# Performance work log

Hardware: AMD Instinct MI355X
Metric: run time of the kernel (lower is better)

The kernel has to match this reference:

```python
import jax, jax.numpy as jnp
import numpy as np

# Model dims (match init_kwargs)
D_MODEL = 512
NUM_EXPERTS = 8
TOP_K = 2
FFN_MULT = 2
HIDDEN = FFN_MULT * D_MODEL
BATCH, SEQ = 4, 2048


def setup_inputs() -> dict:
    key = jax.random.key(0)
    k_x, k_g, k_bg, k_w1, k_w3, k_w2 = jax.random.split(key, 6)
    sd = 1.0 / np.sqrt(D_MODEL).astype(np.float32)
    sh = 1.0 / np.sqrt(HIDDEN).astype(np.float32)
    return {
        "x": jax.random.normal(k_x, (BATCH, SEQ, D_MODEL), dtype=jnp.float32),
        # gate: nn.Linear(d_model, num_experts) with bias
        "Wg": jax.random.normal(k_g, (D_MODEL, NUM_EXPERTS), dtype=jnp.float32) * sd,
        "bg": jax.random.normal(k_bg, (NUM_EXPERTS,), dtype=jnp.float32) * 0.01,
        # stacked per-expert SwiGLU FFN params (no bias, LLaMA-style)
        "W1": jax.random.normal(k_w1, (NUM_EXPERTS, D_MODEL, HIDDEN), dtype=jnp.float32) * sd,
        "W3": jax.random.normal(k_w3, (NUM_EXPERTS, D_MODEL, HIDDEN), dtype=jnp.float32) * sd,
        "W2": jax.random.normal(k_w2, (NUM_EXPERTS, HIDDEN, D_MODEL), dtype=jnp.float32) * sh,
    }


def reference(x, Wg, bg, W1, W3, W2):
    B, S, D = x.shape
    E = Wg.shape[1]
    xt = x.reshape(-1, D)                        # [T, D], T = B*S
    T = xt.shape[0]

    # Router: top-k over experts, softmax over the k selected logits
    logits = xt @ Wg + bg                        # [T, E]
    top_vals, top_idx = jax.lax.top_k(logits, TOP_K)  # [T, K]
    top_probs = jax.nn.softmax(top_vals, axis=-1)     # [T, K]

    # Dense per-(token, expert) combine weight; zero where expert not selected.
    # top-k indices are distinct per token so scatter-add == scatter-set.
    gate_w = jnp.zeros((T, E), dtype=xt.dtype).at[
        jnp.arange(T)[:, None], top_idx
    ].add(top_probs)                              # [T, E]

    # Loop over experts (fixed, small), accumulate weighted expert outputs.
    def body(y, expert):
        w1, w3, w2, g = expert                   # g: [T]
        h = jax.nn.silu(xt @ w1) * (xt @ w3)     # [T, H]
        return y + g[:, None] * (h @ w2), None

    y0 = jnp.zeros_like(xt)
    y, _ = jax.lax.scan(body, y0, (W1, W3, W2, gate_w.T))
    return y.reshape(B, S, D)
```

## Files before the change

kernel.cpp:

```cpp
#include <hip/hip_runtime.h>
#include <hip/hip_bf16.h>

#define TOKENS 8192
#define DM 512
#define NE 8
#define HID 1024
#define NSLOT (TOKENS * 2)
#define NB 32

#define BM 128
#define BN 64
#define BK 64
#define BN2 128
#define MAXTILE 136

typedef __bf16 bf16x8 __attribute__((ext_vector_type(8)));
typedef float floatx4 __attribute__((ext_vector_type(4)));
typedef unsigned short u16x8 __attribute__((ext_vector_type(8)));

__device__ __forceinline__ unsigned short f2bf(float f) {
    union { float f; unsigned u; } c; c.f = f;
    unsigned u = c.u;
    u += 0x7fffu + ((u >> 16) & 1u);
    return (unsigned short)(u >> 16);
}

__device__ __forceinline__ void load16_lds(const void* g, void* l) {
    __builtin_amdgcn_global_load_lds(
        (const __attribute__((address_space(1))) unsigned int*)g,
        (__attribute__((address_space(3))) unsigned int*)l, 16, 0, 0);
}

__global__ void prep_kernel(const float* __restrict__ x, const float* __restrict__ Wg,
                            const float* __restrict__ bg,
                            const float* __restrict__ W1, const float* __restrict__ W3,
                            const float* __restrict__ W2,
                            unsigned short* __restrict__ w1t, unsigned short* __restrict__ w3t,
                            unsigned short* __restrict__ w2t,
                            int* __restrict__ top_idx, float* __restrict__ top_p,
                            unsigned short* __restrict__ xb) {
    if (blockIdx.x < 3072) {
        __shared__ float tile[64][65];
        const int cb = blockIdx.x;
        const int wsel = cb >> 10;
        const float* src; unsigned short* dst; int K, N;
        if (wsel == 0)      { src = W1; dst = w1t; K = DM;  N = HID; }
        else if (wsel == 1) { src = W3; dst = w3t; K = DM;  N = HID; }
        else                { src = W2; dst = w2t; K = HID; N = DM;  }
        const int tkn = (K >> 6) * (N >> 6);
        int b = cb & 1023;
        int e = b / tkn;
        int rem = b % tkn;
        const int tn6 = N >> 6;
        int kt = rem / tn6, nt = rem % tn6;
        int tx = threadIdx.x & 15, ty = threadIdx.x >> 4;
        const float* s = src + ((size_t)(e * K + kt * 64 + ty)) * N + nt * 64 + tx * 4;
        #pragma unroll
        for (int i = 0; i < 4; i++) {
            float4 v = *(const float4*)(s + (size_t)(i * 16) * N);
            float* tr = &tile[ty + i * 16][tx * 4];
            tr[0] = v.x; tr[1] = v.y; tr[2] = v.z; tr[3] = v.w;
        }
        __syncthreads();
        int n = threadIdx.x >> 3;
        int c8 = (threadIdx.x & 7) * 8;
        unsigned short* d = dst + ((size_t)(e * N + nt * 64)) * K + kt * 64;
        #pragma unroll
        for (int i = 0; i < 2; i++) {
            int nn = n + i * 32;
            u16x8 r;
            #pragma unroll
            for (int kk = 0; kk < 8; kk++) r[kk] = f2bf(tile[c8 + kk][nn]);
            *(u16x8*)(d + (size_t)nn * K + c8) = r;
        }
    } else {
        int lane = threadIdx.x & 63, wave = threadIdx.x >> 6;
        int t = (blockIdx.x - 3072) * 4 + wave;
        float acc[NE];
        #pragma unroll
        for (int e = 0; e < NE; e++) acc[e] = 0.f;
        const float* xr = x + (size_t)t * DM;
        unsigned short* xbr = xb + (size_t)t * DM;
        #pragma unroll
        for (int j = 0; j < 8; j++) {
            int d = lane + j * 64;
            float xv = xr[d];
            xbr[d] = f2bf(xv);
            const float4* wr = (const float4*)(Wg + (size_t)d * NE);
            float4 w0 = wr[0], w1 = wr[1];
            acc[0] += xv * w0.x; acc[1] += xv * w0.y; acc[2] += xv * w0.z; acc[3] += xv * w0.w;
            acc[4] += xv * w1.x; acc[5] += xv * w1.y; acc[6] += xv * w1.z; acc[7] += xv * w1.w;
        }
        #pragma unroll
        for (int e = 0; e < NE; e++) {
            float v = acc[e];
            #pragma unroll
            for (int off = 32; off > 0; off >>= 1) v += __shfl_down(v, off, 64);
            acc[e] = v;
        }
        if (lane == 0) {
            float best = -1e30f, second = -1e30f;
            int bi = 0, si = 0;
            #pragma unroll
            for (int e = 0; e < NE; e++) {
                float v = acc[e] + bg[e];
                if (v > best) { second = best; si = bi; best = v; bi = e; }
                else if (v > second) { second = v; si = e; }
            }
            float ex = __expf(second - best);
            float inv = 1.f / (1.f + ex);
            top_idx[t * 2] = bi;  top_idx[t * 2 + 1] = si;
            top_p[t * 2] = inv;   top_p[t * 2 + 1] = ex * inv;
        }
    }
}

__global__ void sortbuild_kernel(const int* __restrict__ top_idx, const float* __restrict__ top_p,
                                 int* __restrict__ counts, int* __restrict__ offsets,
                                 int* __restrict__ rows, float* __restrict__ gates,
                                 int* __restrict__ slot_of) {
    __shared__ int cntAll[NE], cntBef[NE], cur[NE];
    const int b = blockIdx.x, tid = threadIdx.x;
    const int lane = tid & 63;
    if (tid < NE) { cntAll[tid] = 0; cntBef[tid] = 0; }
    __syncthreads();

    unsigned long long aAll = 0ull, aBef = 0ull;
    for (int k = 0; k < TOKENS / 256; k++) {
        int t = k * 256 + tid;
        int2 ei = *(const int2*)(top_idx + (size_t)t * 2);
        unsigned long long inc = (1ull << (ei.x * 8)) + (1ull << (ei.y * 8));
        aAll += inc;
        if (k < b) aBef += inc;
    }
    auto unpackLo = [](unsigned long long a) {
        return ( a        & 0xFFull)        | ((( a >> 8 ) & 0xFFull) << 16)
             | (((a >> 16) & 0xFFull) << 32) | ((( a >> 24) & 0xFFull) << 48);
    };
    auto unpackHi = [](unsigned long long a) {
        return ((a >> 32) & 0xFFull)        | ((( a >> 40) & 0xFFull) << 16)
             | (((a >> 48) & 0xFFull) << 32) | ((( a >> 56) & 0xFFull) << 48);
    };
    unsigned long long sAllLo = unpackLo(aAll), sAllHi = unpackHi(aAll);
    unsigned long long sBefLo = unpackLo(aBef), sBefHi = unpackHi(aBef);
    #pragma unroll
    for (int off = 32; off > 0; off >>= 1) {
        sAllLo += __shfl_down(sAllLo, off, 64);
        sAllHi += __shfl_down(sAllHi, off, 64);
        sBefLo += __shfl_down(sBefLo, off, 64);
        sBefHi += __shfl_down(sBefHi, off, 64);
    }
    if (lane == 0) {
        #pragma unroll
        for (int e = 0; e < 4; e++) {
            atomicAdd(&cntAll[e],     (int)((sAllLo >> (e * 16)) & 0xFFFF));
            atomicAdd(&cntAll[e + 4], (int)((sAllHi >> (e * 16)) & 0xFFFF));
            atomicAdd(&cntBef[e],     (int)((sBefLo >> (e * 16)) & 0xFFFF));
            atomicAdd(&cntBef[e + 4], (int)((sBefHi >> (e * 16)) & 0xFFFF));
        }
    }
    __syncthreads();
    if (tid < NE) {
        int offs = 0;
        for (int ee = 0; ee < tid; ee++) offs += cntAll[ee];
        cur[tid] = offs + cntBef[tid];
        if (b == 0) { counts[tid] = cntAll[tid]; offsets[tid] = offs; }
    }
    __syncthreads();
    const int t = b * 256 + tid;
    #pragma unroll
    for (int k = 0; k < 2; k++) {
        int e = top_idx[t * 2 + k];
        int slot = atomicAdd(&cur[e], 1);
        rows[slot] = t;
        gates[slot] = top_p[t * 2 + k];
        slot_of[t * 2 + k] = slot;
    }
}

__device__ __forceinline__ bool tile_lookup(const int* counts, const int* offsets, int gy,
                                            int& e, int& mt, int& cnt, int& off) {
    int bacc = 0;
    #pragma unroll
    for (int ee = 0; ee < NE; ee++) {
        int c = counts[ee];
        int ntl = (c + BM - 1) >> 7;
        if (gy < bacc + ntl) { e = ee; mt = gy - bacc; cnt = c; off = offsets[ee]; return true; }
        bacc += ntl;
    }
    return false;
}

__global__ __launch_bounds__(256, 4) void gemm1_kernel(
    const unsigned short* __restrict__ xb,
    const unsigned short* __restrict__ w1t,
    const unsigned short* __restrict__ w3t,
    unsigned short* __restrict__ Hb,
    const int* __restrict__ rows, const int* __restrict__ counts,
    const int* __restrict__ offsets) {
    const int lid = blockIdx.x;
    const int xcd = lid & 7;
    const int j = lid >> 3;
    const int gy = xcd * (MAXTILE / 8) + (j >> 4);
    const int nt = j & 15;
    int e, mt, cnt, off;
    if (!tile_lookup(counts, offsets, gy, e, mt, cnt, off)) return;

    __shared__ unsigned short As[BM * BK];
    __shared__ unsigned short B1s[BN * BK];
    __shared__ unsigned short B3s[BN * BK];

    const int tid = threadIdx.x;
    const int lane = tid & 63, wave = tid >> 6;
    const int lrow8 = lane >> 3;
    const int lchunk = (lane & 7) ^ lrow8;

    const unsigned short* a_g[4];
    #pragma unroll
    for (int i = 0; i < 4; i++) {
        int r = (wave * 4 + i) * 8 + lrow8;
        int gr = mt * BM + r;
        int tok = rows[off + (gr < cnt ? gr : 0)];
        a_g[i] = xb + (size_t)tok * DM + lchunk * 8;
    }
    const unsigned short* b1_g[2]; const unsigned short* b3_g[2];
    #pragma unroll
    for (int i = 0; i < 2; i++) {
        int r = (wave * 2 + i) * 8 + lrow8;
        b1_g[i] = w1t + ((size_t)e * HID + nt * BN + r) * DM + lchunk * 8;
        b3_g[i] = w3t + ((size_t)e * HID + nt * BN + r) * DM + lchunk * 8;
    }

    const int l15 = lane & 15, quad = lane >> 4;
    const int sw = l15 & 7;

    floatx4 acc1[2][4], acc3[2][4];
    #pragma unroll
    for (int i = 0; i < 2; i++)
        #pragma unroll
        for (int j2 = 0; j2 < 4; j2++) {
            acc1[i][j2] = (floatx4){0.f, 0.f, 0.f, 0.f};
            acc3[i][j2] = (floatx4){0.f, 0.f, 0.f, 0.f};
        }

    auto stage = [&](int k0) {
        #pragma unroll
        for (int i = 0; i < 4; i++) load16_lds(a_g[i] + k0, &As[(wave * 4 + i) * 512]);
        #pragma unroll
        for (int i = 0; i < 2; i++) {
            load16_lds(b1_g[i] + k0, &B1s[(wave * 2 + i) * 512]);
            load16_lds(b3_g[i] + k0, &B3s[(wave * 2 + i) * 512]);
        }
    };
    auto compute = [&]() {
        #pragma unroll
        for (int kk = 0; kk < 2; kk++) {
            const int qc = kk * 4 + quad;
            const int ch = (qc ^ sw) << 3;
            bf16x8 af[2], bfrag[4];
            #pragma unroll
            for (int mi = 0; mi < 2; mi++)
                af[mi] = *(const bf16x8*)(&As[(wave * 32 + mi * 16 + l15) * 64 + ch]);
            #pragma unroll
            for (int ni = 0; ni < 4; ni++)
                bfrag[ni] = *(const bf16x8*)(&B1s[(ni * 16 + l15) * 64 + ch]);
            #pragma unroll
            for (int mi = 0; mi < 2; mi++)
                #pragma unroll
                for (int ni = 0; ni < 4; ni++)
                    acc1[mi][ni] = __builtin_amdgcn_mfma_f32_16x16x32_bf16(af[mi], bfrag[ni], acc1[mi][ni], 0, 0, 0);
            #pragma unroll
            for (int ni = 0; ni < 4; ni++)
                bfrag[ni] = *(const bf16x8*)(&B3s[(ni * 16 + l15) * 64 + ch]);
            #pragma unroll
            for (int mi = 0; mi < 2; mi++)
                #pragma unroll
                for (int ni = 0; ni < 4; ni++)
                    acc3[mi][ni] = __builtin_amdgcn_mfma_f32_16x16x32_bf16(af[mi], bfrag[ni], acc3[mi][ni], 0, 0, 0);
        }
    };

    const int NI = DM / BK;
    #pragma unroll
    for (int i = 0; i < NI; i++) {
        if (i) __syncthreads();
        stage(i * BK);
        __syncthreads();
        compute();
    }
    #pragma unroll
    for (int mi = 0; mi < 2; mi++) {
        #pragma unroll
        for (int r = 0; r < 4; r++) {
            int mloc = wave * 32 + mi * 16 + quad * 4 + r;
            int gi = mt * BM + mloc;
            if (gi < cnt) {
                size_t rowbase = (size_t)(off + gi) * HID + nt * BN;
                #pragma unroll
                for (int ni = 0; ni < 4; ni++) {
                    float z1 = acc1[mi][ni][r];
                    float z3 = acc3[mi][ni][r];
                    float h = (z1 / (1.f + __expf(-z1))) * z3;
                    Hb[rowbase + ni * 16 + l15] = f2bf(h);
                }
            }
        }
    }
}

__global__ __launch_bounds__(256) void gemm2_kernel(
    const unsigned short* __restrict__ Hb,
    const unsigned short* __restrict__ w2t,
    unsigned short* __restrict__ P,
    const float* __restrict__ gates,
    const int* __restrict__ counts, const int* __restrict__ offsets) {
    const int lid = blockIdx.x;
    const int xcd = lid & 7;
    const int j = lid >> 3;
    const int gy = xcd * (MAXTILE / 8) + (j >> 2);
    const int nt = j & 3;
    int e, mt, cnt, off;
    if (!tile_lookup(counts, offsets, gy, e, mt, cnt, off)) return;

    __shared__ unsigned short As[BM * BK];
    __shared__ unsigned short Bs[BN2 * BK];

    const int tid = threadIdx.x;
    const int lane = tid & 63, wave = tid >> 6;
    const int lrow8 = lane >> 3;
    const int lchunk = (lane & 7) ^ lrow8;

    const unsigned short* a_g[4];
    #pragma unroll
    for (int i = 0; i < 4; i++) {
        int r = (wave * 4 + i) * 8 + lrow8;
        int sl = off + mt * BM + r;
        if (sl >= NSLOT) sl = NSLOT - 1;
        a_g[i] = Hb + (size_t)sl * HID + lchunk * 8;
    }
    const unsigned short* b_g[4];
    #pragma unroll
    for (int i = 0; i < 4; i++) {
        int r = (wave * 4 + i) * 8 + lrow8;
        b_g[i] = w2t + ((size_t)e * DM + nt * BN2 + r) * HID + lchunk * 8;
    }

    const int l15 = lane & 15, quad = lane >> 4;
    const int sw = l15 & 7;

    floatx4 acc[2][8];
    #pragma unroll
    for (int i = 0; i < 2; i++)
        #pragma unroll
        for (int j2 = 0; j2 < 8; j2++) acc[i][j2] = (floatx4){0.f, 0.f, 0.f, 0.f};

    auto stage = [&](int k0) {
        #pragma unroll
        for (int i = 0; i < 4; i++) load16_lds(a_g[i] + k0, &As[(wave * 4 + i) * 512]);
        #pragma unroll
        for (int i = 0; i < 4; i++) load16_lds(b_g[i] + k0, &Bs[(wave * 4 + i) * 512]);
    };
    auto compute = [&]() {
        #pragma unroll
        for (int kk = 0; kk < 2; kk++) {
            const int qc = kk * 4 + quad;
            const int ch = (qc ^ sw) << 3;
            bf16x8 af[2], bf[8];
            #pragma unroll
            for (int mi = 0; mi < 2; mi++)
                af[mi] = *(const bf16x8*)(&As[(wave * 32 + mi * 16 + l15) * 64 + ch]);
            #pragma unroll
            for (int ni = 0; ni < 8; ni++)
                bf[ni] = *(const bf16x8*)(&Bs[(ni * 16 + l15) * 64 + ch]);
            #pragma unroll
            for (int mi = 0; mi < 2; mi++)
                #pragma unroll
                for (int ni = 0; ni < 8; ni++)
                    acc[mi][ni] = __builtin_amdgcn_mfma_f32_16x16x32_bf16(af[mi], bf[ni], acc[mi][ni], 0, 0, 0);
        }
    };

    const int NI = HID / BK;
    #pragma unroll
    for (int i = 0; i < NI; i++) {
        if (i) __syncthreads();
        stage(i * BK);
        __syncthreads();
        compute();
    }
    #pragma unroll
    for (int mi = 0; mi < 2; mi++) {
        #pragma unroll
        for (int r = 0; r < 4; r++) {
            int mloc = wave * 32 + mi * 16 + quad * 4 + r;
            int gi = mt * BM + mloc;
            if (gi < cnt) {
                int slot = off + gi;
                float g = gates[slot];
                #pragma unroll
                for (int ni = 0; ni < 8; ni++) {
                    int col = nt * BN2 + ni * 16 + l15;
                    P[(size_t)slot * DM + col] = f2bf(g * acc[mi][ni][r]);
                }
            }
        }
    }
}

__global__ void combine_kernel(const unsigned short* __restrict__ P,
                               const int* __restrict__ slot_of, float* __restrict__ y) {
    int i = blockIdx.x * blockDim.x + threadIdx.x;
    int t = i / (DM / 8);
    int c8 = i % (DM / 8);
    int s0 = slot_of[t * 2], s1 = slot_of[t * 2 + 1];
    uint4 a = *(const uint4*)(P + (size_t)s0 * DM + c8 * 8);
    uint4 b = *(const uint4*)(P + (size_t)s1 * DM + c8 * 8);
    float o[8];
    const unsigned* aw = (const unsigned*)&a;
    const unsigned* bw = (const unsigned*)&b;
    #pragma unroll
    for (int j = 0; j < 4; j++) {
        union { unsigned u; float f; } al, ah, bl, bh;
        al.u = aw[j] << 16; ah.u = aw[j] & 0xffff0000u;
        bl.u = bw[j] << 16; bh.u = bw[j] & 0xffff0000u;
        o[j * 2]     = al.f + bl.f;
        o[j * 2 + 1] = ah.f + bh.f;
    }
    float4* yo = (float4*)(y + (size_t)t * DM + c8 * 8);
    yo[0] = make_float4(o[0], o[1], o[2], o[3]);
    yo[1] = make_float4(o[4], o[5], o[6], o[7]);
}

extern "C" void kernel_launch(void* const* d_in, const int* in_sizes, int n_in,
                              void* d_out, int out_size, void* d_ws, size_t ws_size,
                              hipStream_t stream) {
    (void)in_sizes; (void)n_in; (void)out_size; (void)ws_size;
    const float* x  = (const float*)d_in[0];
    const float* Wg = (const float*)d_in[1];
    const float* bg = (const float*)d_in[2];
    const float* W1 = (const float*)d_in[3];
    const float* W3 = (const float*)d_in[4];
    const float* W2 = (const float*)d_in[5];
    float* y = (float*)d_out;

    char* p = (char*)d_ws;
    auto carve = [&](size_t bytes) -> char* {
        char* r = p;
        p += (bytes + 255) & ~(size_t)255;
        return r;
    };
    unsigned short* xb   = (unsigned short*)carve((size_t)TOKENS * DM * 2);
    unsigned short* w1t  = (unsigned short*)carve((size_t)NE * DM * HID * 2);
    unsigned short* w3t  = (unsigned short*)carve((size_t)NE * DM * HID * 2);
    unsigned short* w2t  = (unsigned short*)carve((size_t)NE * HID * DM * 2);
    unsigned short* Hb   = (unsigned short*)carve((size_t)NSLOT * HID * 2);
    int*   rows    = (int*)carve(NSLOT * 4);
    float* gates   = (float*)carve(NSLOT * 4);
    int*   slot_of = (int*)carve(NSLOT * 4);
    int*   tidx    = (int*)carve((size_t)TOKENS * 2 * 4);
    float* tp      = (float*)carve((size_t)TOKENS * 2 * 4);
    int*   counts  = (int*)carve(256);
    int*   offsets = (int*)carve(256);
    unsigned short* P = w1t;

    prep_kernel<<<dim3(3072 + TOKENS / 4), dim3(256), 0, stream>>>(
        x, Wg, bg, W1, W3, W2, w1t, w3t, w2t, tidx, tp, xb);
    sortbuild_kernel<<<dim3(NB), dim3(256), 0, stream>>>(
        tidx, tp, counts, offsets, rows, gates, slot_of);
    gemm1_kernel<<<dim3((HID / BN) * MAXTILE), dim3(256), 0, stream>>>(xb, w1t, w3t, Hb, rows, counts, offsets);
    gemm2_kernel<<<dim3((DM / BN2) * MAXTILE), dim3(256), 0, stream>>>(Hb, w2t, P, gates, counts, offsets);
    combine_kernel<<<dim3((TOKENS * DM / 8) / 256), dim3(256), 0, stream>>>(P, slot_of, y);
}
```

Baseline: 196.4 us.

## Fuse top-2 combine into gemm2 epilogue via per-token arrival counters

Removes the separate combine kernel. Each gemm2 block atomically bumps a per-token counter for every row it writes. The block that makes the eighth arrival (4 N-tiles times 2 experts) then reads both bf16 partial rows and writes the fp32 output row. The counters are zeroed in sortbuild. This saves one kernel launch and a full pass over P, at the cost of atomics, threadfences and a serialized combine tail inside gemm2 blocks.

```diff
diff --git a/kernel.cpp b/kernel.cpp
--- a/kernel.cpp
+++ b/kernel.cpp
@@ -118,10 +118,11 @@
 __global__ void sortbuild_kernel(const int* __restrict__ top_idx, const float* __restrict__ top_p,
                                  int* __restrict__ counts, int* __restrict__ offsets,
                                  int* __restrict__ rows, float* __restrict__ gates,
-                                 int* __restrict__ slot_of) {
+                                 int* __restrict__ slot_of, int* __restrict__ ctr) {
     __shared__ int cntAll[NE], cntBef[NE], cur[NE];
     const int b = blockIdx.x, tid = threadIdx.x;
     const int lane = tid & 63;
+    ctr[b * 256 + tid] = 0;
     if (tid < NE) { cntAll[tid] = 0; cntBef[tid] = 0; }
     __syncthreads();
 
@@ -313,6 +314,8 @@
     const unsigned short* __restrict__ w2t,
     unsigned short* __restrict__ P,
     const float* __restrict__ gates,
+    const int* __restrict__ rows, const int* __restrict__ slot_of,
+    int* __restrict__ ctr, float* __restrict__ y,
     const int* __restrict__ counts, const int* __restrict__ offsets) {
     const int lid = blockIdx.x;
     const int xcd = lid & 7;
@@ -324,6 +327,8 @@
 
     __shared__ unsigned short As[BM * BK];
     __shared__ unsigned short Bs[BN2 * BK];
+    __shared__ int nlist;
+    __shared__ int list[BM];
 
     const int tid = threadIdx.x;
     const int lane = tid & 63, wave = tid >> 6;
@@ -388,6 +393,8 @@
         __syncthreads();
         compute();
     }
+    if (tid == 0) nlist = 0;
+    __syncthreads();
     #pragma unroll
     for (int mi = 0; mi < 2; mi++) {
         #pragma unroll
@@ -405,30 +412,49 @@
             }
         }
     }
-}
-
-__global__ void combine_kernel(const unsigned short* __restrict__ P,
-                               const int* __restrict__ slot_of, float* __restrict__ y) {
-    int i = blockIdx.x * blockDim.x + threadIdx.x;
-    int t = i / (DM / 8);
-    int c8 = i % (DM / 8);
-    int s0 = slot_of[t * 2], s1 = slot_of[t * 2 + 1];
-    uint4 a = *(const uint4*)(P + (size_t)s0 * DM + c8 * 8);
-    uint4 b = *(const uint4*)(P + (size_t)s1 * DM + c8 * 8);
-    float o[8];
-    const unsigned* aw = (const unsigned*)&a;
-    const unsigned* bw = (const unsigned*)&b;
-    #pragma unroll
-    for (int j = 0; j < 4; j++) {
-        union { unsigned u; float f; } al, ah, bl, bh;
-        al.u = aw[j] << 16; ah.u = aw[j] & 0xffff0000u;
-        bl.u = bw[j] << 16; bh.u = bw[j] & 0xffff0000u;
-        o[j * 2]     = al.f + bl.f;
-        o[j * 2 + 1] = ah.f + bh.f;
-    }
-    float4* yo = (float4*)(y + (size_t)t * DM + c8 * 8);
-    yo[0] = make_float4(o[0], o[1], o[2], o[3]);
-    yo[1] = make_float4(o[4], o[5], o[6], o[7]);
+    __threadfence();
+    if (l15 == 0) {
+        #pragma unroll
+        for (int mi = 0; mi < 2; mi++) {
+            #pragma unroll
+            for (int r = 0; r < 4; r++) {
+                int mloc = wave * 32 + mi * 16 + quad * 4 + r;
+                int gi = mt * BM + mloc;
+                if (gi < cnt) {
+                    int tok = rows[off + gi] & (TOKENS - 1);
+                    int old = atomicAdd(&ctr[tok], 1);
+                    if (old == 7) {
+                        int ix = atomicAdd(&nlist, 1);
+                        list[ix] = tok;
+                    }
+                }
+            }
+        }
+    }
+    __syncthreads();
+    __threadfence();
+    const int nl = nlist;
+    for (int i = wave; i < nl; i += 4) {
+        int t = list[i];
+        int s0 = slot_of[t * 2] & (NSLOT - 1);
+        int s1 = slot_of[t * 2 + 1] & (NSLOT - 1);
+        uint4 a = *(const uint4*)(P + (size_t)s0 * DM + lane * 8);
+        uint4 b = *(const uint4*)(P + (size_t)s1 * DM + lane * 8);
+        float o[8];
+        const unsigned* aw = (const unsigned*)&a;
+        const unsigned* bw = (const unsigned*)&b;
+        #pragma unroll
+        for (int jj = 0; jj < 4; jj++) {
+            union { unsigned u; float f; } al, ah, bl, bh;
+            al.u = aw[jj] << 16; ah.u = aw[jj] & 0xffff0000u;
+            bl.u = bw[jj] << 16; bh.u = bw[jj] & 0xffff0000u;
+            o[jj * 2]     = al.f + bl.f;
+            o[jj * 2 + 1] = ah.f + bh.f;
+        }
+        float4* yo = (float4*)(y + (size_t)t * DM + lane * 8);
+        yo[0] = make_float4(o[0], o[1], o[2], o[3]);
+        yo[1] = make_float4(o[4], o[5], o[6], o[7]);
+    }
 }
 
 extern "C" void kernel_launch(void* const* d_in, const int* in_sizes, int n_in,
@@ -461,13 +487,14 @@
     float* tp      = (float*)carve((size_t)TOKENS * 2 * 4);
     int*   counts  = (int*)carve(256);
     int*   offsets = (int*)carve(256);
+    int*   ctr     = (int*)carve((size_t)TOKENS * 4);
     unsigned short* P = w1t;
 
     prep_kernel<<<dim3(3072 + TOKENS / 4), dim3(256), 0, stream>>>(
         x, Wg, bg, W1, W3, W2, w1t, w3t, w2t, tidx, tp, xb);
     sortbuild_kernel<<<dim3(NB), dim3(256), 0, stream>>>(
-        tidx, tp, counts, offsets, rows, gates, slot_of);
+        tidx, tp, counts, offsets, rows, gates, slot_of, ctr);
     gemm1_kernel<<<dim3((HID / BN) * MAXTILE), dim3(256), 0, stream>>>(xb, w1t, w3t, Hb, rows, counts, offsets);
-    gemm2_kernel<<<dim3((DM / BN2) * MAXTILE), dim3(256), 0, stream>>>(Hb, w2t, P, gates, counts, offsets);
-    combine_kernel<<<dim3((TOKENS * DM / 8) / 256), dim3(256), 0, stream>>>(P, slot_of, y);
-}
+    gemm2_kernel<<<dim3((DM / BN2) * MAXTILE), dim3(256), 0, stream>>>(
+        Hb, w2t, P, gates, rows, slot_of, ctr, y, counts, offsets);
+}
```

Measured after the change: 347.2 us. 1.77x slower.
